# Optimization experiments

Hardware: AMD Instinct MI355X
Metric: run time of the kernel (lower is better)

## Reference

```python
import jax, jax.numpy as jnp
import numpy as np

EPS = 1e-5
NEG_SLOPE = 0.2

def _bn(h, gamma, beta, axes):
    # training-mode batch norm (batch statistics), matching torch BN forward in train mode
    mu = jnp.mean(h, axis=axes, keepdims=True)
    var = jnp.var(h, axis=axes, keepdims=True)
    return (h - mu) * jax.lax.rsqrt(var + EPS) * gamma + beta

def _lrelu(h):
    return jnp.where(h >= 0, h, NEG_SLOPE * h)

def _edge_conv(x, idx, W, gamma, beta):
    # x: (B,N,C) channels-last; idx: (B,N,k) neighbor indices into N
    # gathered[b,n,j,c] = x[b, idx[b,n,j], c]
    gathered = jnp.take_along_axis(x[:, None, :, :], idx[:, :, :, None], axis=2)  # (B,N,k,C)
    xc = jnp.broadcast_to(x[:, :, None, :], gathered.shape)
    feat = jnp.concatenate([gathered - xc, xc], axis=-1)          # (B,N,k,2C)
    h = jnp.einsum('bnkc,oc->bnko', feat, W)                       # 1x1 conv
    h = _lrelu(_bn(h, gamma, beta, axes=(0, 1, 2)))
    return jnp.max(h, axis=2)                                      # max over k -> (B,N,O)

def setup_inputs() -> dict:
    key = jax.random.key(0)
    ks = jax.random.split(key, 20)
    B, N, K = 8, 2048, 20
    d = {
        'x': jax.random.normal(ks[0], (B, 3, N), jnp.float32),
        'geod_dist': jax.random.normal(ks[1], (B, N, N), jnp.float32),
        'W1': jax.random.normal(ks[2], (64, 6), jnp.float32) * 0.1,
        'g1': jnp.ones((64,)), 'bt1': jnp.zeros((64,)),
        'W2': jax.random.normal(ks[3], (64, 128), jnp.float32) * 0.1,
        'g2': jnp.ones((64,)), 'bt2': jnp.zeros((64,)),
        'W3': jax.random.normal(ks[4], (128, 128), jnp.float32) * 0.1,
        'g3': jnp.ones((128,)), 'bt3': jnp.zeros((128,)),
        'W4': jax.random.normal(ks[5], (256, 256), jnp.float32) * 0.1,
        'g4': jnp.ones((256,)), 'bt4': jnp.zeros((256,)),
        'W5': jax.random.normal(ks[6], (1024, 512), jnp.float32) * 0.05,
        'g5': jnp.ones((1024,)), 'bt5': jnp.zeros((1024,)),
        'L1': jax.random.normal(ks[7], (512, 2048), jnp.float32) * 0.02,
        'g6': jnp.ones((512,)), 'bt6': jnp.zeros((512,)),
        'L2': jax.random.normal(ks[8], (256, 512), jnp.float32) * 0.05,
        'bl2': jnp.zeros((256,)),
        'g7': jnp.ones((256,)), 'bt7': jnp.zeros((256,)),
        'L3': jax.random.normal(ks[9], (40, 256), jnp.float32) * 0.05,
        'bl3': jnp.zeros((40,)),
    }
    return d

def reference(x, geod_dist, W1, g1, bt1, W2, g2, bt2, W3, g3, bt3, W4, g4, bt4,
              W5, g5, bt5, L1, g6, bt6, L2, bl2, g7, bt7, L3, bl3):
    K = 20
    # neighbor indices from geodesic distance (topk largest, as in source)
    idx = jax.lax.top_k(geod_dist, K)[1]            # (B,N,K)
    xt = jnp.transpose(x, (0, 2, 1))                # (B,N,3)
    x1 = _edge_conv(xt, idx, W1, g1, bt1)           # (B,N,64)
    x2 = _edge_conv(x1, idx, W2, g2, bt2)           # (B,N,64)
    x3 = _edge_conv(x2, idx, W3, g3, bt3)           # (B,N,128)
    x4 = _edge_conv(x3, idx, W4, g4, bt4)           # (B,N,256)
    cat = jnp.concatenate([x1, x2, x3, x4], axis=-1)  # (B,N,512)
    h = jnp.einsum('bnc,oc->bno', cat, W5)            # 1x1 conv1d -> (B,N,1024)
    h = _lrelu(_bn(h, g5, bt5, axes=(0, 1)))
    hmax = jnp.max(h, axis=1)                        # (B,1024)
    havg = jnp.mean(h, axis=1)                       # (B,1024)
    z = jnp.concatenate([hmax, havg], axis=1)        # (B,2048)
    z = _lrelu(_bn(z @ L1.T, g6, bt6, axes=(0,)))    # (B,512)
    z = _lrelu(_bn(z @ L2.T + bl2, g7, bt7, axes=(0,)))  # (B,256); dropout = identity (eval)
    return z @ L3.T + bl3                            # (B,40)
```

## Files before the change

### kernel.cpp

```cpp
#include <hip/hip_runtime.h>
#include <hip/hip_bf16.h>
#include <cstdint>
#include <cstddef>

#define NB 8
#define NP 2048
#define NK 20
#define BN 16384

typedef _Float16 half8 __attribute__((ext_vector_type(8)));
typedef float f32x4 __attribute__((ext_vector_type(4)));

__device__ __forceinline__ void gload_lds16(const void* g, void* l) {
  __builtin_amdgcn_global_load_lds(
      (const __attribute__((address_space(1))) unsigned int*)g,
      (__attribute__((address_space(3))) unsigned int*)l, 16, 0, 0);
}

static constexpr size_t OFF_IDX   = 0;
static constexpr size_t OFF_XT    = OFF_IDX + (size_t)BN*NK*4;
static constexpr size_t OFF_XCATH = OFF_XT + (size_t)BN*3*4;
static constexpr size_t OFF_WT1   = OFF_XCATH + (size_t)BN*512*2;
static constexpr size_t OFF_WD1   = OFF_WT1 + 3*64*4;
static constexpr size_t OFF_B2    = OFF_WD1 + 3*64*4;
static constexpr size_t OFF_S2    = OFF_B2 + (size_t)64*64*2;
static constexpr size_t OFF_B3    = OFF_S2 + (size_t)64*64*2;
static constexpr size_t OFF_S3    = OFF_B3 + (size_t)64*128*2;
static constexpr size_t OFF_B4    = OFF_S3 + (size_t)64*128*2;
static constexpr size_t OFF_S4    = OFF_B4 + (size_t)128*256*2;
static constexpr size_t OFF_B5    = OFF_S4 + (size_t)128*256*2;
static constexpr size_t OFF_SBASE = OFF_B5 + (size_t)512*1024*2;
static constexpr size_t OFF_HMAX  = OFF_SBASE + (size_t)BN*256*4;
static constexpr size_t OFF_HMIN  = OFF_HMAX + (size_t)BN*256*4;
static constexpr size_t OFF_H5    = OFF_HMAX;
static constexpr size_t OFF_PART  = OFF_HMIN + (size_t)BN*256*4;
static constexpr size_t OFF_PMEAN = OFF_PART + (size_t)4*1024*1024;
static constexpr size_t OFF_SS    = OFF_PMEAN + (size_t)8*8*1024*4;
static constexpr size_t OFF_Z     = OFF_SS + 2*1024*4;
static constexpr size_t OFF_Z1P   = OFF_Z + (size_t)NB*2048*4;
static constexpr size_t OFF_Z1    = OFF_Z1P + NB*512*4;
static constexpr size_t OFF_Z2P   = OFF_Z1 + NB*512*4;
static constexpr size_t OFF_Z2    = OFF_Z2P + NB*256*4;

__device__ __forceinline__ void prep_b_dev(const float* __restrict__ W,
                                           _Float16* __restrict__ Bp, int t,
                                           int K2, int lgO, int lgRS, bool diff) {
  int O = 1 << lgO;
  int o = t & (O - 1), k = t >> lgO;
  float v;
  if (diff) v = W[((size_t)o << lgRS) + K2 + k] - W[((size_t)o << lgRS) + k];
  else      v = W[((size_t)o << lgRS) + k];
  int ch = k >> 6, ks = (k >> 5) & 1, kg = (k >> 3) & 3, e = k & 7;
  int sl = o >> 4, ol = o & 15;
  size_t flat = (((size_t)(ch * 2 + ks) * (O >> 4) + sl) * 64 + (kg * 16 + ol)) * 8 + e;
  Bp[flat] = (_Float16)v;
}

static constexpr int PB_TR = 0;
static constexpr int PB_W1 = PB_TR + 192;
static constexpr int PB_B2 = PB_W1 + 1;
static constexpr int PB_S2 = PB_B2 + 16;
static constexpr int PB_B3 = PB_S2 + 16;
static constexpr int PB_S3 = PB_B3 + 32;
static constexpr int PB_B4 = PB_S3 + 32;
static constexpr int PB_S4 = PB_B4 + 128;
static constexpr int PB_B5 = PB_S4 + 128;
static constexpr int PB_END = PB_B5 + 2048;

__global__ __launch_bounds__(256) void k_prep_all(
    const float* __restrict__ x, float* __restrict__ xt,
    const float* __restrict__ W1, float* __restrict__ wt1, float* __restrict__ wd1,
    const float* __restrict__ W2, _Float16* __restrict__ b2, _Float16* __restrict__ s2w,
    const float* __restrict__ W3, _Float16* __restrict__ b3, _Float16* __restrict__ s3w,
    const float* __restrict__ W4, _Float16* __restrict__ b4, _Float16* __restrict__ s4w,
    const float* __restrict__ W5, _Float16* __restrict__ b5) {
  int blk = blockIdx.x, tid = threadIdx.x;
  if (blk < PB_W1) {
    int t = blk * 256 + tid;
    int n = t & (NP - 1);
    int c = (t / NP) % 3;
    int b = t / (3 * NP);
    xt[(size_t)(b * NP + n) * 3 + c] = x[t];
  } else if (blk < PB_B2) {
    int t = tid;
    if (t < 192) {
      int o = t & 63, c = t >> 6;
      float w0 = W1[o * 6 + c];
      float w1 = W1[o * 6 + 3 + c];
      wt1[c * 64 + o] = w0;
      wd1[c * 64 + o] = w1 - w0;
    }
  } else if (blk < PB_S2) prep_b_dev(W2, b2,  (blk - PB_B2) * 256 + tid, 64, 6, 7, false);
  else if (blk < PB_B3)   prep_b_dev(W2, s2w, (blk - PB_S2) * 256 + tid, 64, 6, 7, true);
  else if (blk < PB_S3)   prep_b_dev(W3, b3,  (blk - PB_B3) * 256 + tid, 64, 7, 7, false);
  else if (blk < PB_B4)   prep_b_dev(W3, s3w, (blk - PB_S3) * 256 + tid, 64, 7, 7, true);
  else if (blk < PB_S4)   prep_b_dev(W4, b4,  (blk - PB_B4) * 256 + tid, 128, 8, 8, false);
  else if (blk < PB_B5)   prep_b_dev(W4, s4w, (blk - PB_S4) * 256 + tid, 128, 8, 8, true);
  else                    prep_b_dev(W5, b5,  (blk - PB_B5) * 256 + tid, 512, 10, 9, false);
}

template <int CTRL>
__device__ __forceinline__ float dppmax(float x) {
  int t = __builtin_amdgcn_update_dpp(__float_as_int(x), __float_as_int(x),
                                      CTRL, 0xF, 0xF, false);
  return fmaxf(x, __int_as_float(t));
}
template <int CTRL>
__device__ __forceinline__ int dppmin(int x) {
  int t = __builtin_amdgcn_update_dpp(x, x, CTRL, 0xF, 0xF, false);
  return (t < x) ? t : x;
}
__device__ __forceinline__ float wave_max63(float x) {
  x = dppmax<0x111>(x); x = dppmax<0x112>(x); x = dppmax<0x114>(x);
  x = dppmax<0x118>(x); x = dppmax<0x142>(x); x = dppmax<0x143>(x);
  return x;
}
__device__ __forceinline__ int wave_min63(int x) {
  x = dppmin<0x111>(x); x = dppmin<0x112>(x); x = dppmin<0x114>(x);
  x = dppmin<0x118>(x); x = dppmin<0x142>(x); x = dppmin<0x143>(x);
  return x;
}

#define INS3(val, gi, m1, i1, m2, i2, m3, i3)            \
  {                                                      \
    bool c1 = (val) > m1;                                \
    float t_ = c1 ? m1 : (val); int ti_ = c1 ? i1 : (gi);\
    m1 = c1 ? (val) : m1;       i1 = c1 ? (gi) : i1;     \
    bool c2 = t_ > m2;                                   \
    float t2_ = c2 ? m2 : t_;   int t2i_ = c2 ? i2 : ti_;\
    m2 = c2 ? t_ : m2;          i2 = c2 ? ti_ : i2;      \
    bool c3 = t2_ > m3;                                  \
    m3 = c3 ? t2_ : m3;         i3 = c3 ? t2i_ : i3;     \
  }

#define SCAN3(v, m1, i1, m2, i2, m3, i3)                               \
  _Pragma("unroll")                                                    \
  for (int r = 0; r < 8; ++r) {                                        \
    float vals[4] = {v[r].x, v[r].y, v[r].z, v[r].w};                  \
    _Pragma("unroll")                                                  \
    for (int e = 0; e < 4; ++e) {                                      \
      float val = vals[e];                                             \
      int gi = r * 256 + l * 4 + e;                                    \
      INS3(val, gi, m1, i1, m2, i2, m3, i3)                            \
    }                                                                  \
  }

#define SCAN3M(v, dead, m1, i1, m2, i2, m3, i3)                        \
  _Pragma("unroll")                                                    \
  for (int r = 0; r < 8; ++r) {                                        \
    float vals[4] = {v[r].x, v[r].y, v[r].z, v[r].w};                  \
    _Pragma("unroll")                                                  \
    for (int e = 0; e < 4; ++e) {                                      \
      int el = r * 4 + e;                                              \
      float val = ((dead >> el) & 1u) ? NEG : vals[e];                 \
      int gi = r * 256 + l * 4 + e;                                    \
      INS3(val, gi, m1, i1, m2, i2, m3, i3)                            \
    }                                                                  \
  }

__global__ __launch_bounds__(256) void k_topk(const float* __restrict__ geod,
                                              int* __restrict__ idx) {
  int wv = threadIdx.x >> 6, l = threadIdx.x & 63;
  int row = blockIdx.x * 4 + wv;
  const float* g = geod + (size_t)row * NP;
  float4 v[8];
#pragma unroll
  for (int r = 0; r < 8; ++r) v[r] = *(const float4*)&g[r * 256 + l * 4];
  const float NEG = -__builtin_huge_valf();
  unsigned int dead = 0;
  float m1 = NEG, m2 = NEG, m3 = NEG;
  int i1 = 0, i2 = 0, i3 = 0;
  SCAN3(v, m1, i1, m2, i2, m3, i3)
  for (int it = 0; it < NK; ++it) {
    float xr = wave_max63(m1);
    float cv = __int_as_float(__builtin_amdgcn_readlane(__float_as_int(xr), 63));
    int ci = (m1 == cv) ? i1 : (1 << 30);
    ci = wave_min63(ci);
    int best_i = __builtin_amdgcn_readlane(ci, 63);
    if (l == 0) idx[(size_t)row * NK + it] = best_i;
    if (((best_i >> 2) & 63) == l) {
      dead |= 1u << (((best_i >> 8) << 2) | (best_i & 3));
      m1 = m2; i1 = i2; m2 = m3; i2 = i3; m3 = NEG; i3 = 0;
      if (m1 == NEG) { SCAN3M(v, dead, m1, i1, m2, i2, m3, i3) }
    }
  }
}

__global__ __launch_bounds__(256) void k_edge1(
    const float* __restrict__ xt, const int* __restrict__ idx,
    const float* __restrict__ wt1, const float* __restrict__ wd1,
    float* __restrict__ hmax, float* __restrict__ hmin,
    float* __restrict__ part) {
  __shared__ float xl[NP * 3];
  __shared__ int lidx[32 * NK];
  __shared__ float red[256];
  int tid = threadIdx.x;
  int b = blockIdx.x >> 6;
  int grp = blockIdx.x & 63;
  int p0 = grp * 32;
  for (int u = tid; u < NP * 3; u += 256) xl[u] = xt[(size_t)b * NP * 3 + u];
  for (int u = tid; u < 32 * NK; u += 256) lidx[u] = idx[((size_t)b * NP + p0) * NK + u];
  __syncthreads();
  int o = tid & 63;
  int pb = tid >> 6;
  float w0 = wt1[o], w1 = wt1[64 + o], w2 = wt1[128 + o];
  float d0 = wd1[o], d1 = wd1[64 + o], d2 = wd1[128 + o];
  float ps = 0.f, ps2 = 0.f;
#pragma unroll
  for (int i = 0; i < 8; ++i) {
    int pp = pb * 8 + i;
    int p = p0 + pp;
    float base = xl[p * 3] * d0 + xl[p * 3 + 1] * d1 + xl[p * 3 + 2] * d2;
    float mx = -3.4e38f, mn = 3.4e38f;
    for (int j = 0; j < NK; ++j) {
      int nb = lidx[pp * NK + j];
      float h = base + xl[nb * 3] * w0 + xl[nb * 3 + 1] * w1 + xl[nb * 3 + 2] * w2;
      mx = fmaxf(mx, h); mn = fminf(mn, h);
      ps += h; ps2 += h * h;
    }
    size_t P = (size_t)b * NP + p;
    hmax[P * 64 + o] = mx;
    hmin[P * 64 + o] = mn;
  }
  red[tid] = ps;
  __syncthreads();
  if (tid < 64) {
    float a = red[tid] + red[64 + tid] + red[128 + tid] + red[192 + tid];
    part[(size_t)blockIdx.x * 64 + tid] = a;
  }
  __syncthreads();
  red[tid] = ps2;
  __syncthreads();
  if (tid < 64) {
    float a = red[tid] + red[64 + tid] + red[128 + tid] + red[192 + tid];
    part[((size_t)gridDim.x + blockIdx.x) * 64 + tid] = a;
  }
}

template <int C, int O>
__global__ __launch_bounds__(256) void k_self_mfma(
    const _Float16* __restrict__ xh, int in_off,
    const _Float16* __restrict__ Bp, float* __restrict__ sbase) {
  constexpr int NCH = C / 64;
  constexpr int NSLO = O / 16;
  constexpr int NS = NSLO / 2;
  constexpr int PAIRS = 2 * NSLO;
  __shared__ __align__(16) _Float16 ldsA[64 * 64];
  __shared__ __align__(16) _Float16 ldsB[PAIRS * 512];
  int tid = threadIdx.x, wv = tid >> 6, l = tid & 63;
  int m0 = blockIdx.x * 64;
  int mg = wv & 1, ng = wv >> 1;
  f32x4 acc[2][NS];
#pragma unroll
  for (int m = 0; m < 2; ++m)
#pragma unroll
    for (int s = 0; s < NS; ++s)
#pragma unroll
      for (int r = 0; r < 4; ++r) acc[m][s][r] = 0.f;

  for (int ch = 0; ch < NCH; ++ch) {
#pragma unroll
    for (int it = 0; it < 2; ++it) {
      int r0 = wv * 16 + it * 8;
      int R = r0 + (l >> 3);
      int q = (l & 7) ^ (l >> 3);
      gload_lds16(xh + (size_t)(m0 + R) * 512 + in_off + ch * 64 + q * 8, ldsA + r0 * 64);
    }
    for (int u = wv; u < PAIRS; u += 4) {
      int ks = u / NSLO, sloc = u - ks * NSLO;
      gload_lds16(Bp + ((size_t)((ch * 2 + ks) * NSLO + sloc) * 64 + l) * 8,
                  ldsB + u * 512);
    }
    __syncthreads();
#pragma unroll
    for (int ks = 0; ks < 2; ++ks) {
      half8 b[NS];
#pragma unroll
      for (int s = 0; s < NS; ++s)
        b[s] = *(const half8*)(ldsB + (ks * NSLO + ng * NS + s) * 512 + l * 8);
#pragma unroll
      for (int mt = 0; mt < 2; ++mt) {
        int row = mg * 32 + mt * 16 + (l & 15);
        int slot = (ks * 4 + (l >> 4)) ^ (row & 7);
        half8 a = *(const half8*)(ldsA + row * 64 + slot * 8);
#pragma unroll
        for (int s = 0; s < NS; ++s)
          acc[mt][s] = __builtin_amdgcn_mfma_f32_16x16x32_f16(a, b[s], acc[mt][s], 0, 0, 0);
      }
    }
    __syncthreads();
  }
  int g = l >> 4;
#pragma unroll
  for (int s = 0; s < NS; ++s) {
    int col = ng * (NS * 16) + s * 16 + (l & 15);
#pragma unroll
    for (int mt = 0; mt < 2; ++mt)
#pragma unroll
      for (int r = 0; r < 4; ++r) {
        int row = m0 + mg * 32 + mt * 16 + 4 * g + r;
        sbase[(size_t)row * O + col] = acc[mt][s][r];
      }
  }
}

template <int C, int O, int NSPLIT>
__global__ __launch_bounds__(256) void k_edge_mfma(
    const _Float16* __restrict__ xh, int in_off,
    const int* __restrict__ idx,
    const _Float16* __restrict__ Bp, const float* __restrict__ sbase,
    float* __restrict__ hmax, float* __restrict__ hmin,
    float* __restrict__ part) {
  constexpr int NCH = C / 64;
  constexpr int NO = O / NSPLIT;
  constexpr int NSLO = NO / 16;
  constexpr int NS = NSLO / 2;
  constexpr int PAIRS = 2 * NSLO;
  __shared__ __align__(16) _Float16 ldsA[160 * 64];
  __shared__ __align__(16) _Float16 ldsB[PAIRS * 512];
  __shared__ float ldsS[2][NO], ldsQ[2][NO];
  int tid = threadIdx.x, wv = tid >> 6, l = tid & 63;
  int mblk = blockIdx.x, nid = 0;
  if (NSPLIT > 1) { nid = mblk >> 11; mblk &= 2047; }
  int p0 = mblk * 8;
  int bbase = p0 & ~(NP - 1);
  int n_base = nid * NO;
  int mg = wv & 1, ng = wv >> 1;
  f32x4 acc[5][NS];
#pragma unroll
  for (int m = 0; m < 5; ++m)
#pragma unroll
    for (int s = 0; s < NS; ++s)
#pragma unroll
      for (int r = 0; r < 4; ++r) acc[m][s][r] = 0.f;

  for (int ch = 0; ch < NCH; ++ch) {
    int cbase = ch * 64;
#pragma unroll
    for (int it = 0; it < 5; ++it) {
      int r0 = wv * 40 + it * 8;
      int R = r0 + (l >> 3);
      int mgR = R / 80;
      int r = R - mgR * 80;
      int pp = 4 * mgR + ((r >> 2) & 3);
      int j = ((r >> 4) << 2) | (r & 3);
      int p = p0 + pp;
      int srcn = bbase + idx[p * NK + j];
      int q = (l & 7) ^ (l >> 3);
      gload_lds16(xh + (size_t)srcn * 512 + in_off + cbase + q * 8, ldsA + r0 * 64);
    }
    for (int u = wv; u < PAIRS; u += 4) {
      int ks = u / NSLO, sloc = u - ks * NSLO;
      gload_lds16(Bp + ((size_t)((ch * 2 + ks) * (O / 16) + (n_base >> 4) + sloc) * 64 + l) * 8,
                  ldsB + u * 512);
    }
    __syncthreads();
#pragma unroll
    for (int ks = 0; ks < 2; ++ks) {
      half8 b[NS];
#pragma unroll
      for (int s = 0; s < NS; ++s)
        b[s] = *(const half8*)(ldsB + (ks * NSLO + ng * NS + s) * 512 + l * 8);
#pragma unroll
      for (int mt = 0; mt < 5; ++mt) {
        int row = mg * 80 + mt * 16 + (l & 15);
        int slot = (ks * 4 + (l >> 4)) ^ (row & 7);
        half8 a = *(const half8*)(ldsA + row * 64 + slot * 8);
#pragma unroll
        for (int s = 0; s < NS; ++s)
          acc[mt][s] = __builtin_amdgcn_mfma_f32_16x16x32_f16(a, b[s], acc[mt][s], 0, 0, 0);
      }
    }
    __syncthreads();
  }
  int g = l >> 4;
  int p = p0 + 4 * mg + g;
#pragma unroll
  for (int s = 0; s < NS; ++s) {
    int colL = ng * (NS * 16) + s * 16 + (l & 15);
    float sb = sbase[(size_t)p * O + n_base + colL];
    float mx = -3.4e38f, mn = 3.4e38f, sm = 0.f, sq = 0.f;
#pragma unroll
    for (int mt = 0; mt < 5; ++mt)
#pragma unroll
      for (int r = 0; r < 4; ++r) {
        float v = acc[mt][s][r] + sb;
        mx = fmaxf(mx, v); mn = fminf(mn, v); sm += v; sq += v * v;
      }
    hmax[(size_t)p * O + n_base + colL] = mx;
    hmin[(size_t)p * O + n_base + colL] = mn;
    sm += __shfl_xor(sm, 16); sm += __shfl_xor(sm, 32);
    sq += __shfl_xor(sq, 16); sq += __shfl_xor(sq, 32);
    if (l < 16) {
      ldsS[mg][ng * (NS * 16) + s * 16 + l] = sm;
      ldsQ[mg][ng * (NS * 16) + s * 16 + l] = sq;
    }
  }
  __syncthreads();
  for (int u = tid; u < NO; u += 256) {
    part[(size_t)mblk * O + n_base + u] = ldsS[0][u] + ldsS[1][u];
    part[((size_t)2048 + mblk) * O + n_base + u] = ldsQ[0][u] + ldsQ[1][u];
  }
}

__global__ __launch_bounds__(256) void k_conv5_mfma(
    const _Float16* __restrict__ xh, const _Float16* __restrict__ Bp,
    _Float16* __restrict__ h5, float* __restrict__ part) {
  __shared__ __align__(16) _Float16 ldsA[64 * 64];
  __shared__ __align__(16) _Float16 ldsB[32 * 512];
  __shared__ float ldsS[2][256], ldsQ[2][256], ldsMx[2][256], ldsMn[2][256];
  int tid = threadIdx.x, wv = tid >> 6, l = tid & 63;
  int mblk = blockIdx.x & 255, nid = blockIdx.x >> 8;
  int m0 = mblk * 64;
  int n_base = nid * 256;
  int mg = wv & 1, ng = wv >> 1;
  f32x4 acc[2][8];
#pragma unroll
  for (int m = 0; m < 2; ++m)
#pragma unroll
    for (int s = 0; s < 8; ++s)
#pragma unroll
      for (int r = 0; r < 4; ++r) acc[m][s][r] = 0.f;

  for (int ch = 0; ch < 8; ++ch) {
#pragma unroll
    for (int it = 0; it < 2; ++it) {
      int r0 = wv * 16 + it * 8;
      int R = r0 + (l >> 3);
      int q = (l & 7) ^ (l >> 3);
      gload_lds16(xh + (size_t)(m0 + R) * 512 + ch * 64 + q * 8, ldsA + r0 * 64);
    }
    for (int u = wv; u < 32; u += 4) {
      int ks = u >> 4, sloc = u & 15;
      gload_lds16(Bp + ((size_t)((ch * 2 + ks) * 64 + (n_base >> 4) + sloc) * 64 + l) * 8,
                  ldsB + u * 512);
    }
    __syncthreads();
#pragma unroll
    for (int ks = 0; ks < 2; ++ks) {
      half8 b[8];
#pragma unroll
      for (int s = 0; s < 8; ++s)
        b[s] = *(const half8*)(ldsB + (ks * 16 + ng * 8 + s) * 512 + l * 8);
#pragma unroll
      for (int mt = 0; mt < 2; ++mt) {
        int row = mg * 32 + mt * 16 + (l & 15);
        int slot = (ks * 4 + (l >> 4)) ^ (row & 7);
        half8 a = *(const half8*)(ldsA + row * 64 + slot * 8);
#pragma unroll
        for (int s = 0; s < 8; ++s)
          acc[mt][s] = __builtin_amdgcn_mfma_f32_16x16x32_f16(a, b[s], acc[mt][s], 0, 0, 0);
      }
    }
    __syncthreads();
  }
  int g = l >> 4;
#pragma unroll
  for (int s = 0; s < 8; ++s) {
    float sm = 0.f, sq = 0.f, mx = -3.4e38f, mn = 3.4e38f;
    int col = n_base + ng * 128 + s * 16 + (l & 15);
#pragma unroll
    for (int mt = 0; mt < 2; ++mt)
#pragma unroll
      for (int r = 0; r < 4; ++r) {
        float v = acc[mt][s][r];
        int row = m0 + mg * 32 + mt * 16 + 4 * g + r;
        h5[(size_t)row * 1024 + col] = (_Float16)v;
        sm += v; sq += v * v; mx = fmaxf(mx, v); mn = fminf(mn, v);
      }
    sm += __shfl_xor(sm, 16); sm += __shfl_xor(sm, 32);
    sq += __shfl_xor(sq, 16); sq += __shfl_xor(sq, 32);
    mx = fmaxf(mx, __shfl_xor(mx, 16)); mx = fmaxf(mx, __shfl_xor(mx, 32));
    mn = fminf(mn, __shfl_xor(mn, 16)); mn = fminf(mn, __shfl_xor(mn, 32));
    if (l < 16) {
      int u = ng * 128 + s * 16 + l;
      ldsS[mg][u] = sm; ldsQ[mg][u] = sq; ldsMx[mg][u] = mx; ldsMn[mg][u] = mn;
    }
  }
  __syncthreads();
  {
    int u = tid;
    int col = n_base + u;
    part[(size_t)mblk * 1024 + col] = ldsS[0][u] + ldsS[1][u];
    part[((size_t)256 + mblk) * 1024 + col] = ldsQ[0][u] + ldsQ[1][u];
    part[((size_t)512 + mblk) * 1024 + col] = fmaxf(ldsMx[0][u], ldsMx[1][u]);
    part[((size_t)768 + mblk) * 1024 + col] = fminf(ldsMn[0][u], ldsMn[1][u]);
  }
}

__global__ __launch_bounds__(256) void k_finalize(
    const float* __restrict__ part, int G, int O, float inv_count,
    const float* __restrict__ gamma, const float* __restrict__ beta,
    float* __restrict__ ss) {
  int o = blockIdx.x;
  float s = 0.f, s2 = 0.f;
  for (int g = threadIdx.x; g < G; g += 256) {
    s  += part[(size_t)g * O + o];
    s2 += part[((size_t)G + g) * O + o];
  }
#pragma unroll
  for (int sft = 32; sft; sft >>= 1) {
    s  += __shfl_down(s, sft);
    s2 += __shfl_down(s2, sft);
  }
  __shared__ float aw[4], aw2[4];
  int w = threadIdx.x >> 6;
  if ((threadIdx.x & 63) == 0) { aw[w] = s; aw2[w] = s2; }
  __syncthreads();
  if (threadIdx.x == 0) {
    s = aw[0] + aw[1] + aw[2] + aw[3];
    s2 = aw2[0] + aw2[1] + aw2[2] + aw2[3];
    float m   = s * inv_count;
    float var = s2 * inv_count - m * m;
    float scale = gamma[o] * rsqrtf(var + 1e-5f);
    ss[o]     = scale;
    ss[O + o] = beta[o] - m * scale;
  }
}

__global__ void k_edge_apply(const float* __restrict__ hmax, const float* __restrict__ hmin,
                             const float* __restrict__ ss, _Float16* __restrict__ xh,
                             int O, int off) {
  int t = blockIdx.x * 256 + threadIdx.x;
  int o = t % O;
  int p = t / O;
  float scale = ss[o], shift = ss[O + o];
  float v = (scale >= 0.f) ? hmax[t] : hmin[t];
  v = scale * v + shift;
  v = (v >= 0.f) ? v : 0.2f * v;
  xh[(size_t)p * 512 + off + o] = (_Float16)v;
}

__global__ __launch_bounds__(256) void k_pool5a(const _Float16* __restrict__ h5,
                                                const float* __restrict__ ss,
                                                float* __restrict__ pmean) {
  int bi = blockIdx.x;
  int b = bi >> 5, ns = (bi >> 2) & 7, cg = bi & 3;
  int col = cg * 256 + threadIdx.x;
  float scale = ss[col], shift = ss[1024 + col];
  float sm = 0.f;
  for (int n = ns * 256; n < ns * 256 + 256; ++n) {
    float v = (float)h5[(size_t)(b * 2048 + n) * 1024 + col];
    float y = scale * v + shift;
    y = (y >= 0.f) ? y : 0.2f * y;
    sm += y;
  }
  pmean[(size_t)(b * 8 + ns) * 1024 + col] = sm;
}

__global__ __launch_bounds__(256) void k_pool5b(const float* __restrict__ part,
                                                const float* __restrict__ pmean,
                                                const float* __restrict__ ss,
                                                float* __restrict__ z) {
  int bi = blockIdx.x;
  int b = bi >> 2, cg = bi & 3;
  int col = cg * 256 + threadIdx.x;
  float scale = ss[col], shift = ss[1024 + col];
  const float* pmx = part + (size_t)512 * 1024;
  const float* pmn = part + (size_t)768 * 1024;
  float mxh = -3.4e38f, mnh = 3.4e38f;
  for (int q = 0; q < 32; ++q) {
    size_t base = (size_t)(b * 32 + q) * 1024 + col;
    mxh = fmaxf(mxh, pmx[base]);
    mnh = fminf(mnh, pmn[base]);
  }
  float hsel = (scale >= 0.f) ? mxh : mnh;
  float zmax = scale * hsel + shift;
  zmax = (zmax >= 0.f) ? zmax : 0.2f * zmax;
  float sm = 0.f;
  for (int ns = 0; ns < 8; ++ns) sm += pmean[(size_t)(b * 8 + ns) * 1024 + col];
  z[b * 2048 + col] = zmax;
  z[b * 2048 + 1024 + col] = sm * (1.f / 2048.f);
}

__global__ __launch_bounds__(64) void k_fc(const float* __restrict__ in,
                                           const float* __restrict__ Wf,
                                           const float* __restrict__ bias,
                                           float* __restrict__ out, int IN, int O) {
  int blk = blockIdx.x;
  int b = blk / O, o = blk % O;
  const float4* a = (const float4*)(in + (size_t)b * IN);
  const float4* w = (const float4*)(Wf + (size_t)o * IN);
  float s = 0.f;
  for (int i = threadIdx.x; i < (IN >> 2); i += 64) {
    float4 av = a[i], wv = w[i];
    s += av.x * wv.x + av.y * wv.y + av.z * wv.z + av.w * wv.w;
  }
#pragma unroll
  for (int sft = 32; sft; sft >>= 1) s += __shfl_down(s, sft);
  if (threadIdx.x == 0) out[(size_t)b * O + o] = s + (bias ? bias[o] : 0.f);
}

__global__ void k_bn_fc(const float* __restrict__ pre, const float* __restrict__ gamma,
                        const float* __restrict__ beta, float* __restrict__ out, int O) {
  int o = blockIdx.x * 256 + threadIdx.x;
  if (o >= O) return;
  float v[NB];
  float s = 0.f, s2 = 0.f;
#pragma unroll
  for (int b = 0; b < NB; ++b) {
    v[b] = pre[(size_t)b * O + o];
    s += v[b]; s2 += v[b] * v[b];
  }
  float m = s * (1.f / NB);
  float var = s2 * (1.f / NB) - m * m;
  float scale = gamma[o] * rsqrtf(var + 1e-5f);
  float shift = beta[o] - m * scale;
#pragma unroll
  for (int b = 0; b < NB; ++b) {
    float x = scale * v[b] + shift;
    out[(size_t)b * O + o] = (x >= 0.f) ? x : 0.2f * x;
  }
}

extern "C" void kernel_launch(void* const* d_in, const int* in_sizes, int n_in,
                              void* d_out, int out_size, void* d_ws, size_t ws_size,
                              hipStream_t stream) {
  (void)in_sizes; (void)n_in; (void)out_size; (void)ws_size;
  const float* x    = (const float*)d_in[0];
  const float* geod = (const float*)d_in[1];
  const float* W1   = (const float*)d_in[2];
  const float* g1   = (const float*)d_in[3];
  const float* bt1  = (const float*)d_in[4];
  const float* W2   = (const float*)d_in[5];
  const float* g2   = (const float*)d_in[6];
  const float* bt2  = (const float*)d_in[7];
  const float* W3   = (const float*)d_in[8];
  const float* g3   = (const float*)d_in[9];
  const float* bt3  = (const float*)d_in[10];
  const float* W4   = (const float*)d_in[11];
  const float* g4   = (const float*)d_in[12];
  const float* bt4  = (const float*)d_in[13];
  const float* W5   = (const float*)d_in[14];
  const float* g5   = (const float*)d_in[15];
  const float* bt5  = (const float*)d_in[16];
  const float* L1   = (const float*)d_in[17];
  const float* g6   = (const float*)d_in[18];
  const float* bt6  = (const float*)d_in[19];
  const float* L2   = (const float*)d_in[20];
  const float* bl2  = (const float*)d_in[21];
  const float* g7   = (const float*)d_in[22];
  const float* bt7  = (const float*)d_in[23];
  const float* L3   = (const float*)d_in[24];
  const float* bl3  = (const float*)d_in[25];

  char* ws = (char*)d_ws;
  int*       idx   = (int*)(ws + OFF_IDX);
  float*     xt    = (float*)(ws + OFF_XT);
  _Float16*  xcatH = (_Float16*)(ws + OFF_XCATH);
  float*     wt1   = (float*)(ws + OFF_WT1);
  float*     wd1   = (float*)(ws + OFF_WD1);
  _Float16*  b2    = (_Float16*)(ws + OFF_B2);
  _Float16*  s2w   = (_Float16*)(ws + OFF_S2);
  _Float16*  b3    = (_Float16*)(ws + OFF_B3);
  _Float16*  s3w   = (_Float16*)(ws + OFF_S3);
  _Float16*  b4    = (_Float16*)(ws + OFF_B4);
  _Float16*  s4w   = (_Float16*)(ws + OFF_S4);
  _Float16*  b5    = (_Float16*)(ws + OFF_B5);
  float*     sbase = (float*)(ws + OFF_SBASE);
  float*     hmax  = (float*)(ws + OFF_HMAX);
  float*     hmin  = (float*)(ws + OFF_HMIN);
  _Float16*  h5    = (_Float16*)(ws + OFF_H5);
  float*     part  = (float*)(ws + OFF_PART);
  float*     pmean = (float*)(ws + OFF_PMEAN);
  float*     ssb   = (float*)(ws + OFF_SS);
  float*     z     = (float*)(ws + OFF_Z);
  float*     z1p   = (float*)(ws + OFF_Z1P);
  float*     z1    = (float*)(ws + OFF_Z1);
  float*     z2p   = (float*)(ws + OFF_Z2P);
  float*     z2    = (float*)(ws + OFF_Z2);

  const float invE = 1.f / (float)(BN * NK);
  const float inv5 = 1.f / (float)(BN);

  k_prep_all<<<PB_END, 256, 0, stream>>>(x, xt, W1, wt1, wd1,
                                         W2, b2, s2w, W3, b3, s3w,
                                         W4, b4, s4w, W5, b5);
  k_topk<<<BN / 4, 256, 0, stream>>>(geod, idx);

  k_edge1<<<512, 256, 0, stream>>>(xt, idx, wt1, wd1, hmax, hmin, part);
  k_finalize<<<64, 256, 0, stream>>>(part, 512, 64, invE, g1, bt1, ssb);
  k_edge_apply<<<(BN * 64) / 256, 256, 0, stream>>>(hmax, hmin, ssb, xcatH, 64, 0);
  k_self_mfma<64, 64><<<256, 256, 0, stream>>>(xcatH, 0, s2w, sbase);
  k_edge_mfma<64, 64, 1><<<2048, 256, 0, stream>>>(xcatH, 0, idx, b2, sbase, hmax, hmin, part);
  k_finalize<<<64, 256, 0, stream>>>(part, 2048, 64, invE, g2, bt2, ssb);
  k_edge_apply<<<(BN * 64) / 256, 256, 0, stream>>>(hmax, hmin, ssb, xcatH, 64, 64);
  k_self_mfma<64, 128><<<256, 256, 0, stream>>>(xcatH, 64, s3w, sbase);
  k_edge_mfma<64, 128, 1><<<2048, 256, 0, stream>>>(xcatH, 64, idx, b3, sbase, hmax, hmin, part);
  k_finalize<<<128, 256, 0, stream>>>(part, 2048, 128, invE, g3, bt3, ssb);
  k_edge_apply<<<(BN * 128) / 256, 256, 0, stream>>>(hmax, hmin, ssb, xcatH, 128, 128);
  k_self_mfma<128, 256><<<256, 256, 0, stream>>>(xcatH, 128, s4w, sbase);
  k_edge_mfma<128, 256, 2><<<4096, 256, 0, stream>>>(xcatH, 128, idx, b4, sbase, hmax, hmin, part);
  k_finalize<<<256, 256, 0, stream>>>(part, 2048, 256, invE, g4, bt4, ssb);
  k_edge_apply<<<(BN * 256) / 256, 256, 0, stream>>>(hmax, hmin, ssb, xcatH, 256, 256);

  k_conv5_mfma<<<1024, 256, 0, stream>>>(xcatH, b5, h5, part);
  k_finalize<<<1024, 256, 0, stream>>>(part, 256, 1024, inv5, g5, bt5, ssb);
  k_pool5a<<<256, 256, 0, stream>>>(h5, ssb, pmean);
  k_pool5b<<<32, 256, 0, stream>>>(part, pmean, ssb, z);

  k_fc<<<NB * 512, 64, 0, stream>>>(z, L1, nullptr, z1p, 2048, 512);
  k_bn_fc<<<2, 256, 0, stream>>>(z1p, g6, bt6, z1, 512);
  k_fc<<<NB * 256, 64, 0, stream>>>(z1, L2, bl2, z2p, 512, 256);
  k_bn_fc<<<1, 256, 0, stream>>>(z2p, g7, bt7, z2, 256);
  k_fc<<<NB * 40, 64, 0, stream>>>(z2, L3, bl3, (float*)d_out, 256, 40);
}
```

Measured before the change: 261.7 us.

## Precompute per-point projections then gather instead of per-edge MFMA GEMM

Uses linearity of the 1x1 conv: W·[x_j - x_i, x_i] = W_a·x_j + (W_b - W_a)·x_i. Each point's two projections are computed once with a dense MFMA GEMM into a concatenated fp16 buffer. A new gather kernel then adds the neighbor term to the self term and reduces max, min, sum and sum of squares over k. This removes the k-fold redundant GEMM over gathered edges, in exchange for rounding per-point projections to fp16 and a gather of 20 fp16 rows per point. It also changes the partial-statistics layout, with more blocks feeding finalize.

```diff
diff --git a/kernel.cpp b/kernel.cpp
--- a/kernel.cpp
+++ b/kernel.cpp
@@ -9,6 +9,7 @@
 #define BN 16384
 
 typedef _Float16 half8 __attribute__((ext_vector_type(8)));
+typedef _Float16 half4v __attribute__((ext_vector_type(4)));
 typedef float f32x4 __attribute__((ext_vector_type(4)));
 
 __device__ __forceinline__ void gload_lds16(const void* g, void* l) {
@@ -22,19 +23,16 @@
 static constexpr size_t OFF_XCATH = OFF_XT + (size_t)BN*3*4;
 static constexpr size_t OFF_WT1   = OFF_XCATH + (size_t)BN*512*2;
 static constexpr size_t OFF_WD1   = OFF_WT1 + 3*64*4;
-static constexpr size_t OFF_B2    = OFF_WD1 + 3*64*4;
-static constexpr size_t OFF_S2    = OFF_B2 + (size_t)64*64*2;
-static constexpr size_t OFF_B3    = OFF_S2 + (size_t)64*64*2;
-static constexpr size_t OFF_S3    = OFF_B3 + (size_t)64*128*2;
-static constexpr size_t OFF_B4    = OFF_S3 + (size_t)64*128*2;
-static constexpr size_t OFF_S4    = OFF_B4 + (size_t)128*256*2;
-static constexpr size_t OFF_B5    = OFF_S4 + (size_t)128*256*2;
-static constexpr size_t OFF_SBASE = OFF_B5 + (size_t)512*1024*2;
-static constexpr size_t OFF_HMAX  = OFF_SBASE + (size_t)BN*256*4;
+static constexpr size_t OFF_BC2   = OFF_WD1 + 3*64*4;
+static constexpr size_t OFF_BC3   = OFF_BC2 + (size_t)64*128*2;
+static constexpr size_t OFF_BC4   = OFF_BC3 + (size_t)64*256*2;
+static constexpr size_t OFF_B5    = OFF_BC4 + (size_t)128*512*2;
+static constexpr size_t OFF_YH    = OFF_B5 + (size_t)512*1024*2;
+static constexpr size_t OFF_HMAX  = OFF_YH + (size_t)BN*512*2;
 static constexpr size_t OFF_HMIN  = OFF_HMAX + (size_t)BN*256*4;
 static constexpr size_t OFF_H5    = OFF_HMAX;
 static constexpr size_t OFF_PART  = OFF_HMIN + (size_t)BN*256*4;
-static constexpr size_t OFF_PMEAN = OFF_PART + (size_t)4*1024*1024;
+static constexpr size_t OFF_PMEAN = OFF_PART + (size_t)8*1024*1024;
 static constexpr size_t OFF_SS    = OFF_PMEAN + (size_t)8*8*1024*4;
 static constexpr size_t OFF_Z     = OFF_SS + 2*1024*4;
 static constexpr size_t OFF_Z1P   = OFF_Z + (size_t)NB*2048*4;
@@ -44,35 +42,47 @@
 
 __device__ __forceinline__ void prep_b_dev(const float* __restrict__ W,
                                            _Float16* __restrict__ Bp, int t,
-                                           int K2, int lgO, int lgRS, bool diff) {
+                                           int K2, int lgO, int lgRS) {
   int O = 1 << lgO;
   int o = t & (O - 1), k = t >> lgO;
-  float v;
-  if (diff) v = W[((size_t)o << lgRS) + K2 + k] - W[((size_t)o << lgRS) + k];
-  else      v = W[((size_t)o << lgRS) + k];
+  float v = W[((size_t)o << lgRS) + k];
   int ch = k >> 6, ks = (k >> 5) & 1, kg = (k >> 3) & 3, e = k & 7;
   int sl = o >> 4, ol = o & 15;
   size_t flat = (((size_t)(ch * 2 + ks) * (O >> 4) + sl) * 64 + (kg * 16 + ol)) * 8 + e;
   Bp[flat] = (_Float16)v;
 }
 
-static constexpr int PB_TR = 0;
-static constexpr int PB_W1 = PB_TR + 192;
-static constexpr int PB_B2 = PB_W1 + 1;
-static constexpr int PB_S2 = PB_B2 + 16;
-static constexpr int PB_B3 = PB_S2 + 16;
-static constexpr int PB_S3 = PB_B3 + 32;
-static constexpr int PB_B4 = PB_S3 + 32;
-static constexpr int PB_S4 = PB_B4 + 128;
-static constexpr int PB_B5 = PB_S4 + 128;
+__device__ __forceinline__ void prep_bc_dev(const float* __restrict__ W,
+                                            _Float16* __restrict__ Bp, int t,
+                                            int C, int lgO2, int lgRS) {
+  int O2 = 1 << lgO2, O = O2 >> 1;
+  int o2 = t & (O2 - 1), k = t >> lgO2;
+  float v;
+  if (o2 < O) v = W[((size_t)o2 << lgRS) + k];
+  else {
+    int o = o2 - O;
+    v = W[((size_t)o << lgRS) + C + k] - W[((size_t)o << lgRS) + k];
+  }
+  int ch = k >> 6, ks = (k >> 5) & 1, kg = (k >> 3) & 3, e = k & 7;
+  int sl = o2 >> 4, ol = o2 & 15;
+  size_t flat = (((size_t)(ch * 2 + ks) * (O2 >> 4) + sl) * 64 + (kg * 16 + ol)) * 8 + e;
+  Bp[flat] = (_Float16)v;
+}
+
+static constexpr int PB_TR  = 0;
+static constexpr int PB_W1  = PB_TR + 192;
+static constexpr int PB_BC2 = PB_W1 + 1;
+static constexpr int PB_BC3 = PB_BC2 + 32;
+static constexpr int PB_BC4 = PB_BC3 + 64;
+static constexpr int PB_B5  = PB_BC4 + 256;
 static constexpr int PB_END = PB_B5 + 2048;
 
 __global__ __launch_bounds__(256) void k_prep_all(
     const float* __restrict__ x, float* __restrict__ xt,
     const float* __restrict__ W1, float* __restrict__ wt1, float* __restrict__ wd1,
-    const float* __restrict__ W2, _Float16* __restrict__ b2, _Float16* __restrict__ s2w,
-    const float* __restrict__ W3, _Float16* __restrict__ b3, _Float16* __restrict__ s3w,
-    const float* __restrict__ W4, _Float16* __restrict__ b4, _Float16* __restrict__ s4w,
+    const float* __restrict__ W2, _Float16* __restrict__ bc2,
+    const float* __restrict__ W3, _Float16* __restrict__ bc3,
+    const float* __restrict__ W4, _Float16* __restrict__ bc4,
     const float* __restrict__ W5, _Float16* __restrict__ b5) {
   int blk = blockIdx.x, tid = threadIdx.x;
   if (blk < PB_W1) {
@@ -81,7 +91,7 @@
     int c = (t / NP) % 3;
     int b = t / (3 * NP);
     xt[(size_t)(b * NP + n) * 3 + c] = x[t];
-  } else if (blk < PB_B2) {
+  } else if (blk < PB_BC2) {
     int t = tid;
     if (t < 192) {
       int o = t & 63, c = t >> 6;
@@ -90,13 +100,10 @@
       wt1[c * 64 + o] = w0;
       wd1[c * 64 + o] = w1 - w0;
     }
-  } else if (blk < PB_S2) prep_b_dev(W2, b2,  (blk - PB_B2) * 256 + tid, 64, 6, 7, false);
-  else if (blk < PB_B3)   prep_b_dev(W2, s2w, (blk - PB_S2) * 256 + tid, 64, 6, 7, true);
-  else if (blk < PB_S3)   prep_b_dev(W3, b3,  (blk - PB_B3) * 256 + tid, 64, 7, 7, false);
-  else if (blk < PB_B4)   prep_b_dev(W3, s3w, (blk - PB_S3) * 256 + tid, 64, 7, 7, true);
-  else if (blk < PB_S4)   prep_b_dev(W4, b4,  (blk - PB_B4) * 256 + tid, 128, 8, 8, false);
-  else if (blk < PB_B5)   prep_b_dev(W4, s4w, (blk - PB_S4) * 256 + tid, 128, 8, 8, true);
-  else                    prep_b_dev(W5, b5,  (blk - PB_B5) * 256 + tid, 512, 10, 9, false);
+  } else if (blk < PB_BC3) prep_bc_dev(W2, bc2, (blk - PB_BC2) * 256 + tid, 64, 7, 7);
+  else if (blk < PB_BC4)   prep_bc_dev(W3, bc3, (blk - PB_BC3) * 256 + tid, 64, 8, 7);
+  else if (blk < PB_B5)    prep_bc_dev(W4, bc4, (blk - PB_BC4) * 256 + tid, 128, 9, 8);
+  else                     prep_b_dev(W5, b5,   (blk - PB_B5) * 256 + tid, 512, 10, 9);
 }
 
 template <int CTRL>
@@ -237,18 +244,22 @@
   }
 }
 
-template <int C, int O>
-__global__ __launch_bounds__(256) void k_self_mfma(
+template <int C, int O2, int NSPLIT>
+__global__ __launch_bounds__(256) void k_dense_mfma(
     const _Float16* __restrict__ xh, int in_off,
-    const _Float16* __restrict__ Bp, float* __restrict__ sbase) {
+    const _Float16* __restrict__ Bp, _Float16* __restrict__ yH) {
   constexpr int NCH = C / 64;
-  constexpr int NSLO = O / 16;
+  constexpr int NO = O2 / NSPLIT;
+  constexpr int NSLO = NO / 16;
   constexpr int NS = NSLO / 2;
   constexpr int PAIRS = 2 * NSLO;
   __shared__ __align__(16) _Float16 ldsA[64 * 64];
   __shared__ __align__(16) _Float16 ldsB[PAIRS * 512];
   int tid = threadIdx.x, wv = tid >> 6, l = tid & 63;
-  int m0 = blockIdx.x * 64;
+  int mblk = blockIdx.x, nid = 0;
+  if (NSPLIT > 1) { nid = mblk >> 8; mblk &= 255; }
+  int m0 = mblk * 64;
+  int n_base = nid * NO;
   int mg = wv & 1, ng = wv >> 1;
   f32x4 acc[2][NS];
 #pragma unroll
@@ -268,7 +279,7 @@
     }
     for (int u = wv; u < PAIRS; u += 4) {
       int ks = u / NSLO, sloc = u - ks * NSLO;
-      gload_lds16(Bp + ((size_t)((ch * 2 + ks) * NSLO + sloc) * 64 + l) * 8,
+      gload_lds16(Bp + ((size_t)((ch * 2 + ks) * (O2 / 16) + (n_base >> 4) + sloc) * 64 + l) * 8,
                   ldsB + u * 512);
     }
     __syncthreads();
@@ -293,113 +304,64 @@
   int g = l >> 4;
 #pragma unroll
   for (int s = 0; s < NS; ++s) {
-    int col = ng * (NS * 16) + s * 16 + (l & 15);
+    int col = n_base + ng * (NS * 16) + s * 16 + (l & 15);
 #pragma unroll
     for (int mt = 0; mt < 2; ++mt)
 #pragma unroll
       for (int r = 0; r < 4; ++r) {
         int row = m0 + mg * 32 + mt * 16 + 4 * g + r;
-        sbase[(size_t)row * O + col] = acc[mt][s][r];
+        yH[(size_t)row * O2 + col] = (_Float16)acc[mt][s][r];
       }
   }
 }
 
-template <int C, int O, int NSPLIT>
-__global__ __launch_bounds__(256) void k_edge_mfma(
-    const _Float16* __restrict__ xh, int in_off,
-    const int* __restrict__ idx,
-    const _Float16* __restrict__ Bp, const float* __restrict__ sbase,
+template <int O>
+__global__ __launch_bounds__(256) void k_gather(
+    const _Float16* __restrict__ yH, const int* __restrict__ idx,
     float* __restrict__ hmax, float* __restrict__ hmin,
     float* __restrict__ part) {
-  constexpr int NCH = C / 64;
-  constexpr int NO = O / NSPLIT;
-  constexpr int NSLO = NO / 16;
-  constexpr int NS = NSLO / 2;
-  constexpr int PAIRS = 2 * NSLO;
-  __shared__ __align__(16) _Float16 ldsA[160 * 64];
-  __shared__ __align__(16) _Float16 ldsB[PAIRS * 512];
-  __shared__ float ldsS[2][NO], ldsQ[2][NO];
-  int tid = threadIdx.x, wv = tid >> 6, l = tid & 63;
-  int mblk = blockIdx.x, nid = 0;
-  if (NSPLIT > 1) { nid = mblk >> 11; mblk &= 2047; }
-  int p0 = mblk * 8;
+  constexpr int O2 = 2 * O;
+  constexpr int CG = O / 4;
+  constexpr int PPB = 256 / CG;
+  __shared__ int lidx[PPB * NK];
+  __shared__ float4 redS[256], redQ[256];
+  int tid = threadIdx.x;
+  int p0 = blockIdx.x * PPB;
   int bbase = p0 & ~(NP - 1);
-  int n_base = nid * NO;
-  int mg = wv & 1, ng = wv >> 1;
-  f32x4 acc[5][NS];
-#pragma unroll
-  for (int m = 0; m < 5; ++m)
-#pragma unroll
-    for (int s = 0; s < NS; ++s)
-#pragma unroll
-      for (int r = 0; r < 4; ++r) acc[m][s][r] = 0.f;
-
-  for (int ch = 0; ch < NCH; ++ch) {
-    int cbase = ch * 64;
-#pragma unroll
-    for (int it = 0; it < 5; ++it) {
-      int r0 = wv * 40 + it * 8;
-      int R = r0 + (l >> 3);
-      int mgR = R / 80;
-      int r = R - mgR * 80;
-      int pp = 4 * mgR + ((r >> 2) & 3);
-      int j = ((r >> 4) << 2) | (r & 3);
-      int p = p0 + pp;
-      int srcn = bbase + idx[p * NK + j];
-      int q = (l & 7) ^ (l >> 3);
-      gload_lds16(xh + (size_t)srcn * 512 + in_off + cbase + q * 8, ldsA + r0 * 64);
-    }
-    for (int u = wv; u < PAIRS; u += 4) {
-      int ks = u / NSLO, sloc = u - ks * NSLO;
-      gload_lds16(Bp + ((size_t)((ch * 2 + ks) * (O / 16) + (n_base >> 4) + sloc) * 64 + l) * 8,
-                  ldsB + u * 512);
-    }
-    __syncthreads();
-#pragma unroll
-    for (int ks = 0; ks < 2; ++ks) {
-      half8 b[NS];
-#pragma unroll
-      for (int s = 0; s < NS; ++s)
-        b[s] = *(const half8*)(ldsB + (ks * NSLO + ng * NS + s) * 512 + l * 8);
-#pragma unroll
-      for (int mt = 0; mt < 5; ++mt) {
-        int row = mg * 80 + mt * 16 + (l & 15);
-        int slot = (ks * 4 + (l >> 4)) ^ (row & 7);
-        half8 a = *(const half8*)(ldsA + row * 64 + slot * 8);
-#pragma unroll
-        for (int s = 0; s < NS; ++s)
-          acc[mt][s] = __builtin_amdgcn_mfma_f32_16x16x32_f16(a, b[s], acc[mt][s], 0, 0, 0);
-      }
-    }
-    __syncthreads();
-  }
-  int g = l >> 4;
-  int p = p0 + 4 * mg + g;
-#pragma unroll
-  for (int s = 0; s < NS; ++s) {
-    int colL = ng * (NS * 16) + s * 16 + (l & 15);
-    float sb = sbase[(size_t)p * O + n_base + colL];
-    float mx = -3.4e38f, mn = 3.4e38f, sm = 0.f, sq = 0.f;
-#pragma unroll
-    for (int mt = 0; mt < 5; ++mt)
-#pragma unroll
-      for (int r = 0; r < 4; ++r) {
-        float v = acc[mt][s][r] + sb;
-        mx = fmaxf(mx, v); mn = fminf(mn, v); sm += v; sq += v * v;
-      }
-    hmax[(size_t)p * O + n_base + colL] = mx;
-    hmin[(size_t)p * O + n_base + colL] = mn;
-    sm += __shfl_xor(sm, 16); sm += __shfl_xor(sm, 32);
-    sq += __shfl_xor(sq, 16); sq += __shfl_xor(sq, 32);
-    if (l < 16) {
-      ldsS[mg][ng * (NS * 16) + s * 16 + l] = sm;
-      ldsQ[mg][ng * (NS * 16) + s * 16 + l] = sq;
-    }
-  }
-  __syncthreads();
-  for (int u = tid; u < NO; u += 256) {
-    part[(size_t)mblk * O + n_base + u] = ldsS[0][u] + ldsS[1][u];
-    part[((size_t)2048 + mblk) * O + n_base + u] = ldsQ[0][u] + ldsQ[1][u];
+  for (int u = tid; u < PPB * NK; u += 256) lidx[u] = idx[(size_t)p0 * NK + u];
+  __syncthreads();
+  int pp = tid / CG, g = tid - pp * CG;
+  int p = p0 + pp;
+  half4v sb4 = *(const half4v*)&yH[(size_t)p * O2 + O + g * 4];
+  float sb[4] = {(float)sb4[0], (float)sb4[1], (float)sb4[2], (float)sb4[3]};
+  float mx[4], mn[4], sm[4], sq[4];
+#pragma unroll
+  for (int e = 0; e < 4; ++e) { mx[e] = -3.4e38f; mn[e] = 3.4e38f; sm[e] = 0.f; sq[e] = 0.f; }
+#pragma unroll
+  for (int j = 0; j < NK; ++j) {
+    int nb = bbase + lidx[pp * NK + j];
+    half4v y4 = *(const half4v*)&yH[(size_t)nb * O2 + g * 4];
+#pragma unroll
+    for (int e = 0; e < 4; ++e) {
+      float h = (float)y4[e] + sb[e];
+      mx[e] = fmaxf(mx[e], h); mn[e] = fminf(mn[e], h);
+      sm[e] += h; sq[e] += h * h;
+    }
+  }
+  *(float4*)&hmax[(size_t)p * O + g * 4] = make_float4(mx[0], mx[1], mx[2], mx[3]);
+  *(float4*)&hmin[(size_t)p * O + g * 4] = make_float4(mn[0], mn[1], mn[2], mn[3]);
+  redS[tid] = make_float4(sm[0], sm[1], sm[2], sm[3]);
+  redQ[tid] = make_float4(sq[0], sq[1], sq[2], sq[3]);
+  __syncthreads();
+  if (tid < CG) {
+    float4 a = redS[tid], q = redQ[tid];
+    for (int k = 1; k < PPB; ++k) {
+      float4 b = redS[tid + k * CG], c = redQ[tid + k * CG];
+      a.x += b.x; a.y += b.y; a.z += b.z; a.w += b.w;
+      q.x += c.x; q.y += c.y; q.z += c.z; q.w += c.w;
+    }
+    *(float4*)&part[(size_t)blockIdx.x * O + tid * 4] = a;
+    *(float4*)&part[((size_t)gridDim.x + blockIdx.x) * O + tid * 4] = q;
   }
 }
 
@@ -650,14 +612,11 @@
   _Float16*  xcatH = (_Float16*)(ws + OFF_XCATH);
   float*     wt1   = (float*)(ws + OFF_WT1);
   float*     wd1   = (float*)(ws + OFF_WD1);
-  _Float16*  b2    = (_Float16*)(ws + OFF_B2);
-  _Float16*  s2w   = (_Float16*)(ws + OFF_S2);
-  _Float16*  b3    = (_Float16*)(ws + OFF_B3);
-  _Float16*  s3w   = (_Float16*)(ws + OFF_S3);
-  _Float16*  b4    = (_Float16*)(ws + OFF_B4);
-  _Float16*  s4w   = (_Float16*)(ws + OFF_S4);
+  _Float16*  bc2   = (_Float16*)(ws + OFF_BC2);
+  _Float16*  bc3   = (_Float16*)(ws + OFF_BC3);
+  _Float16*  bc4   = (_Float16*)(ws + OFF_BC4);
   _Float16*  b5    = (_Float16*)(ws + OFF_B5);
-  float*     sbase = (float*)(ws + OFF_SBASE);
+  _Float16*  yH    = (_Float16*)(ws + OFF_YH);
   float*     hmax  = (float*)(ws + OFF_HMAX);
   float*     hmin  = (float*)(ws + OFF_HMIN);
   _Float16*  h5    = (_Float16*)(ws + OFF_H5);
@@ -674,24 +633,23 @@
   const float inv5 = 1.f / (float)(BN);
 
   k_prep_all<<<PB_END, 256, 0, stream>>>(x, xt, W1, wt1, wd1,
-                                         W2, b2, s2w, W3, b3, s3w,
-                                         W4, b4, s4w, W5, b5);
+                                         W2, bc2, W3, bc3, W4, bc4, W5, b5);
   k_topk<<<BN / 4, 256, 0, stream>>>(geod, idx);
 
   k_edge1<<<512, 256, 0, stream>>>(xt, idx, wt1, wd1, hmax, hmin, part);
   k_finalize<<<64, 256, 0, stream>>>(part, 512, 64, invE, g1, bt1, ssb);
   k_edge_apply<<<(BN * 64) / 256, 256, 0, stream>>>(hmax, hmin, ssb, xcatH, 64, 0);
-  k_self_mfma<64, 64><<<256, 256, 0, stream>>>(xcatH, 0, s2w, sbase);
-  k_edge_mfma<64, 64, 1><<<2048, 256, 0, stream>>>(xcatH, 0, idx, b2, sbase, hmax, hmin, part);
-  k_finalize<<<64, 256, 0, stream>>>(part, 2048, 64, invE, g2, bt2, ssb);
+  k_dense_mfma<64, 128, 1><<<256, 256, 0, stream>>>(xcatH, 0, bc2, yH);
+  k_gather<64><<<BN / 16, 256, 0, stream>>>(yH, idx, hmax, hmin, part);
+  k_finalize<<<64, 256, 0, stream>>>(part, BN / 16, 64, invE, g2, bt2, ssb);
   k_edge_apply<<<(BN * 64) / 256, 256, 0, stream>>>(hmax, hmin, ssb, xcatH, 64, 64);
-  k_self_mfma<64, 128><<<256, 256, 0, stream>>>(xcatH, 64, s3w, sbase);
-  k_edge_mfma<64, 128, 1><<<2048, 256, 0, stream>>>(xcatH, 64, idx, b3, sbase, hmax, hmin, part);
-  k_finalize<<<128, 256, 0, stream>>>(part, 2048, 128, invE, g3, bt3, ssb);
+  k_dense_mfma<64, 256, 1><<<256, 256, 0, stream>>>(xcatH, 64, bc3, yH);
+  k_gather<128><<<BN / 8, 256, 0, stream>>>(yH, idx, hmax, hmin, part);
+  k_finalize<<<128, 256, 0, stream>>>(part, BN / 8, 128, invE, g3, bt3, ssb);
   k_edge_apply<<<(BN * 128) / 256, 256, 0, stream>>>(hmax, hmin, ssb, xcatH, 128, 128);
-  k_self_mfma<128, 256><<<256, 256, 0, stream>>>(xcatH, 128, s4w, sbase);
-  k_edge_mfma<128, 256, 2><<<4096, 256, 0, stream>>>(xcatH, 128, idx, b4, sbase, hmax, hmin, part);
-  k_finalize<<<256, 256, 0, stream>>>(part, 2048, 256, invE, g4, bt4, ssb);
+  k_dense_mfma<128, 512, 2><<<512, 256, 0, stream>>>(xcatH, 128, bc4, yH);
+  k_gather<256><<<BN / 4, 256, 0, stream>>>(yH, idx, hmax, hmin, part);
+  k_finalize<<<256, 256, 0, stream>>>(part, BN / 4, 256, invE, g4, bt4, ssb);
   k_edge_apply<<<(BN * 256) / 256, 256, 0, stream>>>(hmax, hmin, ssb, xcatH, 256, 256);
 
   k_conv5_mfma<<<1024, 256, 0, stream>>>(xcatH, b5, h5, part);
```

Measured after the change: 243.3 us. 1.08x faster.
